# Performance work log

Hardware: AMD Instinct MI355X
Metric: run time of the kernel (lower is better)

## Reference

```python
import jax, jax.numpy as jnp
import numpy as np

D = 2048
H = 16
HD = D // H


def setup_inputs() -> dict:
    key = jax.random.key(0)
    k1, k2, k3 = jax.random.split(key, 3)
    x = jax.random.normal(k1, (2, 2048, D), dtype=jnp.float32)
    # torch Linear(d, 3d, bias=False): y = x @ W.T; store transposed weight [D, 3D]
    Wqkv = jax.random.normal(k2, (D, 3 * D), dtype=jnp.float32) * (D ** -0.5)
    Wo = jax.random.normal(k3, (D, D), dtype=jnp.float32) * (D ** -0.5)
    return {"x": x, "Wqkv": Wqkv, "Wo": Wo}


def reference(x, Wqkv, Wo):
    B, S, _ = x.shape
    qkv = (x @ Wqkv).reshape(B, S, 3, H, HD)
    q = qkv[:, :, 0].transpose(0, 2, 1, 3)  # [B,H,S,HD]
    k = qkv[:, :, 1].transpose(0, 2, 1, 3)
    v = qkv[:, :, 2].transpose(0, 2, 1, 3)
    scores = jnp.einsum("bhqd,bhkd->bhqk", q, k) * (HD ** -0.5)
    causal = jnp.tril(jnp.ones((S, S), dtype=bool))  # keep lower triangle
    scores = jnp.where(causal, scores, jnp.float32(-1e9))
    a = jax.nn.softmax(scores, axis=-1)
    o = jnp.einsum("bhqk,bhkd->bhqd", a, v)
    o = o.transpose(0, 2, 1, 3).reshape(B, S, H * HD)
    return o @ Wo
```

## Files before the change

kernel.cpp:

```cpp
#include <hip/hip_runtime.h>
#include <hip/hip_bf16.h>
#include <cstdint>

typedef __bf16 bf16;
typedef __bf16 bf16x8 __attribute__((ext_vector_type(8)));
typedef __bf16 bf16x4 __attribute__((ext_vector_type(4)));
typedef float floatx4 __attribute__((ext_vector_type(4)));

#define MFMA16(a, b, c) __builtin_amdgcn_mfma_f32_16x16x32_bf16(a, b, c, 0, 0, 0)

__device__ __forceinline__ void gload_lds16(const void* g, void* l) {
    __builtin_amdgcn_global_load_lds(
        (const __attribute__((address_space(1))) void*)g,
        (__attribute__((address_space(3))) void*)l, 16, 0, 0);
}

__global__ void downcast_kernel(const float* __restrict__ in, bf16* __restrict__ out,
                                size_t n) {
    const size_t i = ((size_t)blockIdx.x * blockDim.x + threadIdx.x) * 4;
    if (i >= n) return;
    const float4 v = *(const float4*)(in + i);
    bf16x4 o = {(bf16)v.x, (bf16)v.y, (bf16)v.z, (bf16)v.w};
    *(bf16x4*)(out + i) = o;
}

__global__ void transpose_kernel(const float* __restrict__ in, bf16* __restrict__ out,
                                 int R, int C) {
    __shared__ float tile[32][33];
    const int c0 = blockIdx.x * 32, r0 = blockIdx.y * 32;
    const int tx = threadIdx.x & 31, ty = threadIdx.x >> 5;
    for (int i = 0; i < 32; i += 8)
        tile[ty + i][tx] = in[(size_t)(r0 + ty + i) * C + (c0 + tx)];
    __syncthreads();
    for (int i = 0; i < 32; i += 8)
        out[(size_t)(c0 + ty + i) * R + (r0 + tx)] = (bf16)tile[tx][ty + i];
}

template <int MODE>
__global__ __launch_bounds__(256) void gemm_bt_kernel(
    const bf16* __restrict__ A, const bf16* __restrict__ BT,
    int M, int N, int K,
    bf16* __restrict__ qt, bf16* __restrict__ kt, bf16* __restrict__ vt,
    float* __restrict__ Cout) {
    __shared__ alignas(16) bf16 As[128 * 64];
    __shared__ alignas(16) bf16 Bs[128 * 64];

    const int tid = threadIdx.x;
    const int wave = tid >> 6, lane = tid & 63;
    const int quad = lane >> 4, r16 = lane & 15;
    const int m0 = blockIdx.y * 128, n0 = blockIdx.x * 128;
    const int wm = (wave >> 1) * 64, wn = (wave & 1) * 64;

    int srow[4], soff[4];
#pragma unroll
    for (int j = 0; j < 4; ++j) {
        const int c = tid + j * 256;
        srow[j] = c >> 3;
        soff[j] = ((c & 7) ^ (srow[j] & 7)) * 8;
    }

    floatx4 acc[4][4] = {};

    for (int k0 = 0; k0 < K; k0 += 64) {
        __syncthreads();
#pragma unroll
        for (int j = 0; j < 4; ++j) {
            const int c = tid + j * 256;
            gload_lds16(A + (size_t)(m0 + srow[j]) * K + k0 + soff[j], As + c * 8);
            gload_lds16(BT + (size_t)(n0 + srow[j]) * K + k0 + soff[j], Bs + c * 8);
        }
        __syncthreads();

#pragma unroll
        for (int kc = 0; kc < 2; ++kc) {
            bf16x8 a[4], b[4];
#pragma unroll
            for (int i = 0; i < 4; ++i) {
                const int row = wm + i * 16 + r16;
                const int sp = (4 * kc + quad) ^ (row & 7);
                a[i] = *(const bf16x8*)(As + row * 64 + sp * 8);
            }
#pragma unroll
            for (int j = 0; j < 4; ++j) {
                const int row = wn + j * 16 + r16;
                const int sp = (4 * kc + quad) ^ (row & 7);
                b[j] = *(const bf16x8*)(Bs + row * 64 + sp * 8);
            }
#pragma unroll
            for (int i = 0; i < 4; ++i)
#pragma unroll
                for (int j = 0; j < 4; ++j)
                    acc[i][j] = MFMA16(a[i], b[j], acc[i][j]);
        }
    }

    if (MODE == 0) {
        const int t = n0 >> 11;
        const float qscale = 0.08838834764831845f;
#pragma unroll
        for (int i = 0; i < 4; ++i) {
            const int mbase = m0 + wm + i * 16 + quad * 4;
            const int b_ = mbase >> 11;
            const int s = mbase & 2047;
#pragma unroll
            for (int j = 0; j < 4; ++j) {
                const int n = n0 + wn + j * 16 + r16;
                const int h = (n >> 7) & 15, hd = n & 127;
                const int bh = b_ * 16 + h;
                if (t == 0) {
#pragma unroll
                    for (int r = 0; r < 4; ++r)
                        qt[(size_t)(bh * 2048 + s + r) * 128 + hd] =
                            (bf16)(acc[i][j][r] * qscale);
                } else if (t == 1) {
#pragma unroll
                    for (int r = 0; r < 4; ++r)
                        kt[(size_t)(bh * 2048 + s + r) * 128 + hd] = (bf16)acc[i][j][r];
                } else {
                    bf16x4 pv = {(bf16)acc[i][j][0], (bf16)acc[i][j][1],
                                 (bf16)acc[i][j][2], (bf16)acc[i][j][3]};
                    *(bf16x4*)(vt + (size_t)(bh * 128 + hd) * 2048 + s) = pv;
                }
            }
        }
    } else {
#pragma unroll
        for (int i = 0; i < 4; ++i) {
            const int mbase = m0 + wm + i * 16 + quad * 4;
#pragma unroll
            for (int j = 0; j < 4; ++j) {
                const int n = n0 + wn + j * 16 + r16;
#pragma unroll
                for (int r = 0; r < 4; ++r)
                    Cout[(size_t)(mbase + r) * N + n] = acc[i][j][r];
            }
        }
    }
}

__global__ __launch_bounds__(256) void attn_kernel(
    const bf16* __restrict__ qt, const bf16* __restrict__ kt,
    const bf16* __restrict__ vt, bf16* __restrict__ o) {
    __shared__ alignas(16) bf16 Ks[64 * 128];
    __shared__ alignas(16) bf16 Vts[128 * 64];
    __shared__ alignas(16) bf16 Ps[4][16 * 72];

    const int tid = threadIdx.x;
    const int wave = tid >> 6, lane = tid & 63;
    const int quad = lane >> 4, r16 = lane & 15;
    const int pair = blockIdx.x, bh = blockIdx.y;
    const int b_ = bh >> 4, h = bh & 15;

    for (int half = 0; half < 2; ++half) {
        const int t = half == 0 ? pair : 31 - pair;
        const int q0 = t * 64;

        bf16x8 aq[4];
        {
            const bf16* qbase = qt + (((size_t)bh * 2048 + q0 + wave * 16 + r16) << 7);
#pragma unroll
            for (int kc = 0; kc < 4; ++kc)
                aq[kc] = *(const bf16x8*)(qbase + kc * 32 + quad * 8);
        }

        floatx4 oacc[8] = {};
        float lsum[4] = {0.f, 0.f, 0.f, 0.f};

        for (int it = 0; it <= t; ++it) {
            const int k0 = it * 64;
            __syncthreads();
#pragma unroll
            for (int j = 0; j < 4; ++j) {
                const int c = tid + j * 256;
                const int row = c >> 4, sp = c & 15, s = sp ^ (row & 15);
                gload_lds16(kt + (((size_t)bh * 2048 + k0 + row) << 7) + s * 8,
                            Ks + c * 8);
            }
#pragma unroll
            for (int j = 0; j < 4; ++j) {
                const int c = tid + j * 256;
                const int row = c >> 3, sp = c & 7, s = sp ^ (row & 7);
                gload_lds16(vt + ((size_t)bh * 128 + row) * 2048 + k0 + s * 8,
                            Vts + c * 8);
            }
            __syncthreads();

            floatx4 sacc[4] = {};
#pragma unroll
            for (int nt = 0; nt < 4; ++nt) {
                const int row = nt * 16 + r16;
#pragma unroll
                for (int kc = 0; kc < 4; ++kc) {
                    const int sp = (4 * kc + quad) ^ r16;
                    bf16x8 bk = *(const bf16x8*)(Ks + row * 128 + sp * 8);
                    sacc[nt] = MFMA16(aq[kc], bk, sacc[nt]);
                }
            }

            const int qrowC = q0 + wave * 16 + quad * 4;
            float p[4][4];
            if (it == t) {
#pragma unroll
                for (int nt = 0; nt < 4; ++nt)
#pragma unroll
                    for (int r = 0; r < 4; ++r) {
                        const bool ok = (k0 + nt * 16 + r16) <= (qrowC + r);
                        const float e = ok ? __expf(sacc[nt][r]) : 0.f;
                        p[nt][r] = e;
                        lsum[r] += e;
                    }
            } else {
#pragma unroll
                for (int nt = 0; nt < 4; ++nt)
#pragma unroll
                    for (int r = 0; r < 4; ++r) {
                        const float e = __expf(sacc[nt][r]);
                        p[nt][r] = e;
                        lsum[r] += e;
                    }
            }

#pragma unroll
            for (int nt = 0; nt < 4; ++nt)
#pragma unroll
                for (int r = 0; r < 4; ++r)
                    Ps[wave][(quad * 4 + r) * 72 + nt * 16 + r16] = (bf16)p[nt][r];

#pragma unroll
            for (int kblk = 0; kblk < 2; ++kblk) {
                bf16x8 ap = *(const bf16x8*)(&Ps[wave][r16 * 72 + kblk * 32 + quad * 8]);
#pragma unroll
                for (int nt2 = 0; nt2 < 8; ++nt2) {
                    const int row = nt2 * 16 + r16;
                    const int sp = (4 * kblk + quad) ^ (row & 7);
                    bf16x8 bv = *(const bf16x8*)(Vts + row * 64 + sp * 8);
                    oacc[nt2] = MFMA16(ap, bv, oacc[nt2]);
                }
            }
        }

#pragma unroll
        for (int r = 0; r < 4; ++r) {
            float s = lsum[r];
#pragma unroll
            for (int off = 1; off < 16; off <<= 1) s += __shfl_xor(s, off);
            lsum[r] = s;
        }

#pragma unroll
        for (int r = 0; r < 4; ++r) {
            const int qq = q0 + wave * 16 + quad * 4 + r;
            const float inv = 1.0f / lsum[r];
            bf16* orow = o + (size_t)(b_ * 2048 + qq) * 2048 + h * 128;
#pragma unroll
            for (int nt2 = 0; nt2 < 8; ++nt2)
                orow[nt2 * 16 + r16] = (bf16)(oacc[nt2][r] * inv);
        }
    }
}

extern "C" void kernel_launch(void* const* d_in, const int* in_sizes, int n_in,
                              void* d_out, int out_size, void* d_ws, size_t ws_size,
                              hipStream_t stream) {
    const float* x    = (const float*)d_in[0];
    const float* Wqkv = (const float*)d_in[1];
    const float* Wo   = (const float*)d_in[2];
    float* out        = (float*)d_out;

    char* ws = (char*)d_ws;
    bf16* xb    = (bf16*)ws; ws += (size_t)4096 * 2048 * 2;
    bf16* WqkvT = (bf16*)ws; ws += (size_t)6144 * 2048 * 2;
    bf16* WoT   = (bf16*)ws; ws += (size_t)2048 * 2048 * 2;
    bf16* qt    = (bf16*)ws; ws += (size_t)32 * 2048 * 128 * 2;
    bf16* kt    = (bf16*)ws; ws += (size_t)32 * 2048 * 128 * 2;
    bf16* vt    = (bf16*)ws; ws += (size_t)32 * 128 * 2048 * 2;
    bf16* ob    = (bf16*)ws; ws += (size_t)4096 * 2048 * 2;

    downcast_kernel<<<8192, 256, 0, stream>>>(x, xb, (size_t)4096 * 2048);
    transpose_kernel<<<dim3(192, 64), 256, 0, stream>>>(Wqkv, WqkvT, 2048, 6144);
    transpose_kernel<<<dim3(64, 64), 256, 0, stream>>>(Wo, WoT, 2048, 2048);

    gemm_bt_kernel<0><<<dim3(48, 32), 256, 0, stream>>>(
        xb, WqkvT, 4096, 6144, 2048, qt, kt, vt, nullptr);

    attn_kernel<<<dim3(16, 32), 256, 0, stream>>>(qt, kt, vt, ob);

    gemm_bt_kernel<1><<<dim3(16, 32), 256, 0, stream>>>(
        ob, WoT, 4096, 2048, 2048, nullptr, nullptr, nullptr, out);
}
```

Baseline: 380.4 us.

## Replace QKV projection GEMM with 256x256-tile double-buffered 8-wave kernel

Adds a dedicated QKV GEMM kernel that uses 256x256 output tiles with 512 threads, double-buffered LDS staging through direct global-to-LDS loads, and a four-phase interleaving of LDS reads, prefetch and MFMA with raised wave priority. It also remaps blocks with a swizzle so neighbouring blocks share operands in cache. The larger tile is meant to raise arithmetic intensity and hide load latency compared with the previous 128x128 kernel. In exchange it uses 128KB of LDS and many accumulator registers, which limits occupancy to one block per CU. The 384-block grid is also close to the CU count, so wave quantization may cost something.

```diff
diff --git a/kernel.cpp b/kernel.cpp
--- a/kernel.cpp
+++ b/kernel.cpp
@@ -14,6 +14,9 @@
         (const __attribute__((address_space(1))) void*)g,
         (__attribute__((address_space(3))) void*)l, 16, 0, 0);
 }
+
+#define BARRIER()    asm volatile("s_barrier" ::: "memory")
+#define WAIT_LGKM0() asm volatile("s_waitcnt lgkmcnt(0)" ::: "memory")
 
 __global__ void downcast_kernel(const float* __restrict__ in, bf16* __restrict__ out,
                                 size_t n) {
@@ -36,6 +39,179 @@
         out[(size_t)(c0 + ty + i) * R + (r0 + tx)] = (bf16)tile[tx][ty + i];
 }
 
+__global__ __launch_bounds__(512) void gemm256_qkv_kernel(
+    const bf16* __restrict__ A, const bf16* __restrict__ BT, int K,
+    bf16* __restrict__ qt, bf16* __restrict__ kt, bf16* __restrict__ vt) {
+    __shared__ alignas(16) bf16 As[2][16384];
+    __shared__ alignas(16) bf16 Bs[2][16384];
+
+    const int tid = threadIdx.x;
+    const int wave = tid >> 6, lane = tid & 63;
+    const int quad = lane >> 4, r16 = lane & 15;
+
+    const int flat = blockIdx.y * 24 + blockIdx.x;
+    const int swz = (flat & 7) * 48 + (flat >> 3);
+    const int n0 = (swz % 24) << 8, m0 = (swz / 24) << 8;
+
+    const int wm = (wave >> 2) << 7;
+    const int wn = (wave & 3) << 6;
+
+    int srow[2], soff[2];
+#pragma unroll
+    for (int j = 0; j < 2; ++j) {
+        const int c = tid + j * 512;
+        srow[j] = c >> 3;
+        soff[j] = ((c & 7) ^ (srow[j] & 7)) * 8;
+    }
+
+    const int NT = K >> 6;
+
+    auto stageA = [&](int bufi, int hf, int kt_) {
+#pragma unroll
+        for (int j = 0; j < 2; ++j) {
+            const int c = tid + j * 512;
+            gload_lds16(A + (size_t)(m0 + hf * 128 + srow[j]) * K + (kt_ << 6) + soff[j],
+                        &As[bufi][hf * 8192 + c * 8]);
+        }
+    };
+    auto stageB = [&](int bufi, int hf, int kt_) {
+#pragma unroll
+        for (int j = 0; j < 2; ++j) {
+            const int c = tid + j * 512;
+            gload_lds16(BT + (size_t)(n0 + hf * 128 + srow[j]) * K + (kt_ << 6) + soff[j],
+                        &Bs[bufi][hf * 8192 + c * 8]);
+        }
+    };
+
+    floatx4 acc[8][4] = {};
+
+    stageA(0, 0, 0); stageA(0, 1, 0);
+    stageB(0, 0, 0); stageB(0, 1, 0);
+    stageA(1, 0, 1); stageA(1, 1, 1);
+    asm volatile("s_waitcnt vmcnt(4)" ::: "memory");
+    BARRIER();
+
+    for (int t = 0; t < NT; ++t) {
+        const int bsel = t & 1;
+        const bf16* Ab = &As[bsel][0];
+        const bf16* Bb = &Bs[bsel][0];
+        bf16x8 alo[4][2], ahi[4][2], blo[2][2], bhi[2][2];
+
+#pragma unroll
+        for (int i = 0; i < 4; ++i) {
+            const int row = wm + i * 16 + r16;
+#pragma unroll
+            for (int kc = 0; kc < 2; ++kc)
+                alo[i][kc] = *(const bf16x8*)(Ab + row * 64 + ((4 * kc + quad) ^ (row & 7)) * 8);
+        }
+#pragma unroll
+        for (int j = 0; j < 2; ++j) {
+            const int row = wn + j * 16 + r16;
+#pragma unroll
+            for (int kc = 0; kc < 2; ++kc)
+                blo[j][kc] = *(const bf16x8*)(Bb + row * 64 + ((4 * kc + quad) ^ (row & 7)) * 8);
+        }
+        if (t + 1 < NT) stageB(bsel ^ 1, 0, t + 1);
+        BARRIER();
+        WAIT_LGKM0();
+        __builtin_amdgcn_s_setprio(1);
+#pragma unroll
+        for (int i = 0; i < 4; ++i)
+#pragma unroll
+            for (int j = 0; j < 2; ++j)
+#pragma unroll
+                for (int kc = 0; kc < 2; ++kc)
+                    acc[i][j] = MFMA16(alo[i][kc], blo[j][kc], acc[i][j]);
+        __builtin_amdgcn_s_setprio(0);
+        BARRIER();
+
+#pragma unroll
+        for (int j = 0; j < 2; ++j) {
+            const int row = wn + (2 + j) * 16 + r16;
+#pragma unroll
+            for (int kc = 0; kc < 2; ++kc)
+                bhi[j][kc] = *(const bf16x8*)(Bb + row * 64 + ((4 * kc + quad) ^ (row & 7)) * 8);
+        }
+        if (t + 1 < NT) stageB(bsel ^ 1, 1, t + 1);
+        BARRIER();
+        WAIT_LGKM0();
+        __builtin_amdgcn_s_setprio(1);
+#pragma unroll
+        for (int i = 0; i < 4; ++i)
+#pragma unroll
+            for (int j = 0; j < 2; ++j)
+#pragma unroll
+                for (int kc = 0; kc < 2; ++kc)
+                    acc[i][2 + j] = MFMA16(alo[i][kc], bhi[j][kc], acc[i][2 + j]);
+        __builtin_amdgcn_s_setprio(0);
+        BARRIER();
+
+#pragma unroll
+        for (int i = 0; i < 4; ++i) {
+            const int row = wm + (4 + i) * 16 + r16;
+#pragma unroll
+            for (int kc = 0; kc < 2; ++kc)
+                ahi[i][kc] = *(const bf16x8*)(Ab + row * 64 + ((4 * kc + quad) ^ (row & 7)) * 8);
+        }
+        BARRIER();
+        WAIT_LGKM0();
+        __builtin_amdgcn_s_setprio(1);
+#pragma unroll
+        for (int i = 0; i < 4; ++i)
+#pragma unroll
+            for (int j = 0; j < 2; ++j)
+#pragma unroll
+                for (int kc = 0; kc < 2; ++kc)
+                    acc[4 + i][2 + j] = MFMA16(ahi[i][kc], bhi[j][kc], acc[4 + i][2 + j]);
+        __builtin_amdgcn_s_setprio(0);
+        BARRIER();
+
+        if (t + 2 < NT) { stageA(bsel, 0, t + 2); stageA(bsel, 1, t + 2); }
+        BARRIER();
+        __builtin_amdgcn_s_setprio(1);
+#pragma unroll
+        for (int i = 0; i < 4; ++i)
+#pragma unroll
+            for (int j = 0; j < 2; ++j)
+#pragma unroll
+                for (int kc = 0; kc < 2; ++kc)
+                    acc[4 + i][j] = MFMA16(ahi[i][kc], blo[j][kc], acc[4 + i][j]);
+        __builtin_amdgcn_s_setprio(0);
+        if (t + 2 < NT) asm volatile("s_waitcnt vmcnt(4)" ::: "memory");
+        else            asm volatile("s_waitcnt vmcnt(0)" ::: "memory");
+        BARRIER();
+    }
+
+    const int tsel = n0 >> 11;
+    const float qscale = 0.08838834764831845f;
+#pragma unroll
+    for (int i = 0; i < 8; ++i) {
+        const int mbase = m0 + wm + i * 16 + quad * 4;
+        const int b_ = mbase >> 11;
+        const int s = mbase & 2047;
+#pragma unroll
+        for (int j = 0; j < 4; ++j) {
+            const int n = n0 + wn + j * 16 + r16;
+            const int h = (n >> 7) & 15, hd = n & 127;
+            const int bh = b_ * 16 + h;
+            if (tsel == 0) {
+#pragma unroll
+                for (int r = 0; r < 4; ++r)
+                    qt[(size_t)(bh * 2048 + s + r) * 128 + hd] =
+                        (bf16)(acc[i][j][r] * qscale);
+            } else if (tsel == 1) {
+#pragma unroll
+                for (int r = 0; r < 4; ++r)
+                    kt[(size_t)(bh * 2048 + s + r) * 128 + hd] = (bf16)acc[i][j][r];
+            } else {
+                bf16x4 pv = {(bf16)acc[i][j][0], (bf16)acc[i][j][1],
+                             (bf16)acc[i][j][2], (bf16)acc[i][j][3]};
+                *(bf16x4*)(vt + (size_t)(bh * 128 + hd) * 2048 + s) = pv;
+            }
+        }
+    }
+}
+
 template <int MODE>
 __global__ __launch_bounds__(256) void gemm_bt_kernel(
     const bf16* __restrict__ A, const bf16* __restrict__ BT,
@@ -280,8 +456,8 @@
     transpose_kernel<<<dim3(192, 64), 256, 0, stream>>>(Wqkv, WqkvT, 2048, 6144);
     transpose_kernel<<<dim3(64, 64), 256, 0, stream>>>(Wo, WoT, 2048, 2048);
 
-    gemm_bt_kernel<0><<<dim3(48, 32), 256, 0, stream>>>(
-        xb, WqkvT, 4096, 6144, 2048, qt, kt, vt, nullptr);
+    gemm256_qkv_kernel<<<dim3(24, 16), 512, 0, stream>>>(
+        xb, WqkvT, 2048, qt, kt, vt);
 
     attn_kernel<<<dim3(16, 32), 256, 0, stream>>>(qt, kt, vt, ob);
 
```

New measurement: 389.8 us. 2.5% more time.
